# Kernel optimization log

Measured on AMD Instinct MI355X. Metric: run time of the kernel, lower is better.

## Reference

```python
import jax, jax.numpy as jnp
import numpy as np

B, N, M = 2, 2048, 2048
D_K, D_V, H = 256, 256, 8
D_KS = D_K // H  # 32, per-head key dim (ceil(256/8))
D_VS = D_V // H  # 32
MASK_BIG = 1e32


def setup_inputs() -> dict:
    key = jax.random.key(0)
    ks = jax.random.split(key, 10)
    s = 0.02
    queries = jax.random.normal(ks[0], (B, N, D_K), jnp.float32)
    keys_ = jax.random.normal(ks[1], (B, M, D_K), jnp.float32)
    values = jax.random.normal(ks[2], (B, M, D_V), jnp.float32)
    presence = (jax.random.uniform(ks[3], (B, M)) > 0.3).astype(jnp.float32)
    Wq = jax.random.normal(ks[4], (D_K, D_KS * H), jnp.float32) * s
    bq = jnp.zeros((D_KS * H,), jnp.float32)
    Wk = jax.random.normal(ks[5], (D_K, D_KS * H), jnp.float32) * s
    bk = jnp.zeros((D_KS * H,), jnp.float32)
    Wv = jax.random.normal(ks[6], (D_V, D_VS * H), jnp.float32) * s
    bv = jnp.zeros((D_VS * H,), jnp.float32)
    Wo = jax.random.normal(ks[7], (D_VS * H, D_V), jnp.float32) * s
    bo = jnp.zeros((D_V,), jnp.float32)
    return {"queries": queries, "keys": keys_, "values": values, "presence": presence,
            "Wq": Wq, "bq": bq, "Wk": Wk, "bk": bk, "Wv": Wv, "bv": bv, "Wo": Wo, "bo": bo}


def reference(queries, keys, values, presence, Wq, bq, Wk, bk, Wv, bv, Wo, bo):
    # Project and split into heads. torch's split(d_k_s,-1)+cat(...,0) puts the
    # head index as the outer batch dim; a [B,N,H,d] reshape is the same math.
    q = (queries @ Wq + bq).reshape(B, N, H, D_KS)
    k = (keys @ Wk + bk).reshape(B, M, H, D_KS)
    v = (values @ Wv + bv).reshape(B, M, H, D_VS)
    # Raw scores, additive presence mask, then scale by sqrt(per-head d_k)
    scores = jnp.einsum('bnhd,bmhd->bhnm', q, k)
    scores = scores - (1.0 - presence)[:, None, None, :] * MASK_BIG
    attn = jax.nn.softmax(scores / np.sqrt(D_KS).astype(np.float32), axis=-1)
    o = jnp.einsum('bhnm,bmhd->bnhd', attn, v).reshape(B, N, H * D_VS)
    return o @ Wo + bo
```

## Files before the change

### kernel.cpp

```cpp
#include <hip/hip_runtime.h>

#define B_ 2
#define N_ 2048
#define M_ 2048
#define D_ 256
#define H_ 8
#define DH_ 32
#define SPLITS 2
#define QSCALE (0.17677669529663689f * 1.4426950408889634f)

typedef __attribute__((ext_vector_type(8))) short short8;
typedef __attribute__((ext_vector_type(4))) float f32x4;
typedef unsigned short u16;
typedef unsigned int u32;

#if __has_builtin(__builtin_amdgcn_exp2f)
#define EXP2 __builtin_amdgcn_exp2f
#else
#define EXP2 exp2f
#endif

__device__ __forceinline__ u16 f2bf(float f) {
  u32 u = __float_as_uint(f);
  return (u16)((u + 0x7fffu + ((u >> 16) & 1u)) >> 16);
}
__device__ __forceinline__ u32 cvtpk_bf16(float lo, float hi) {
  u32 r;
  asm("v_cvt_pk_bf16_f32 %0, %1, %2" : "=v"(r) : "v"(lo), "v"(hi));
  return r;
}
__device__ __forceinline__ void gload_lds16(const u16* g, u16* l) {
  __builtin_amdgcn_global_load_lds((const __attribute__((address_space(1))) void*)g,
                                   (__attribute__((address_space(3))) void*)l, 16, 0, 0);
}

__global__ __launch_bounds__(256, 2) void qkvproj_kernel(
    const float* __restrict__ Xq, const float* __restrict__ Xk, const float* __restrict__ Xv,
    const float* __restrict__ Wq, const float* __restrict__ Wk, const float* __restrict__ Wv,
    const float* __restrict__ bq, const float* __restrict__ bk, const float* __restrict__ bv,
    u16* __restrict__ qb, u16* __restrict__ kb, u16* __restrict__ vtb) {
  __shared__ u16 wsT[64 * 256];
  __shared__ u16 xs[64 * 256];
  const int p = blockIdx.y;
  const int nb = blockIdx.x & 63, cb = blockIdx.x >> 6;
  const int n0B = nb * 64, c0B = cb * 64;
  const float* X = p == 0 ? Xq : (p == 1 ? Xk : Xv);
  const float* W = p == 0 ? Wq : (p == 1 ? Wk : Wv);
  const float* bias = p == 0 ? bq : (p == 1 ? bk : bv);
  const int t = threadIdx.x;

  {
    const int cL = (t & 15) * 4, kB = (t >> 4) * 16;
    const float* wp = W + (size_t)kB * D_ + c0B + cL;
#pragma unroll
    for (int u = 0; u < 4; ++u) {
      const int k0 = kB + 4 * u;
      const f32x4 w0 = *(const f32x4*)(wp + (size_t)(4 * u + 0) * D_);
      const f32x4 w1 = *(const f32x4*)(wp + (size_t)(4 * u + 1) * D_);
      const f32x4 w2 = *(const f32x4*)(wp + (size_t)(4 * u + 2) * D_);
      const f32x4 w3 = *(const f32x4*)(wp + (size_t)(4 * u + 3) * D_);
#pragma unroll
      for (int cc = 0; cc < 4; ++cc) {
        const int c = cL + cc;
        uint2 v;
        v.x = cvtpk_bf16(w0[cc], w1[cc]);
        v.y = cvtpk_bf16(w2[cc], w3[cc]);
        *(uint2*)(wsT + c * 256 + (((k0 >> 3) ^ (c & 7)) * 8) + (k0 & 7)) = v;
      }
    }
  }
  {
    const int nL = t >> 2, k64 = (t & 3) * 64;
    const float* xp = X + (size_t)(n0B + nL) * D_ + k64;
#pragma unroll
    for (int m = 0; m < 8; ++m) {
      const f32x4 a = *(const f32x4*)(xp + 8 * m);
      const f32x4 b = *(const f32x4*)(xp + 8 * m + 4);
      uint4 v;
      v.x = cvtpk_bf16(a[0], a[1]);
      v.y = cvtpk_bf16(a[2], a[3]);
      v.z = cvtpk_bf16(b[0], b[1]);
      v.w = cvtpk_bf16(b[2], b[3]);
      const int k0 = k64 + 8 * m;
      *(uint4*)(xs + nL * 256 + (((k0 >> 3) ^ (nL & 7)) * 8)) = v;
    }
  }
  __syncthreads();

  const int wv = t >> 6, lane = t & 63, lr = lane & 15, lg = lane >> 4;
  const f32x4 zz = {0.f, 0.f, 0.f, 0.f};
  f32x4 acc[4] = {zz, zz, zz, zz};
  const int arow = wv * 16 + lr;
#pragma unroll
  for (int ks = 0; ks < 8; ++ks) {
    const short8 a = *(const short8*)(wsT + arow * 256 + (((ks * 4 + lg) ^ (arow & 7)) * 8));
#pragma unroll
    for (int ng = 0; ng < 4; ++ng) {
      const int brow = ng * 16 + lr;
      const short8 b = *(const short8*)(xs + brow * 256 + (((ks * 4 + lg) ^ (brow & 7)) * 8));
      acc[ng] = __builtin_amdgcn_mfma_f32_16x16x32_bf16(a, b, acc[ng], 0, 0, 0);
    }
  }

  const int cg4 = c0B + wv * 16 + lg * 4;
  const f32x4 bias4 = *(const f32x4*)(bias + cg4);
  if (p < 2) {
    u16* ob = p == 0 ? qb : kb;
    const float sc = p == 0 ? QSCALE : 1.0f;
#pragma unroll
    for (int ng = 0; ng < 4; ++ng) {
      const int n = n0B + ng * 16 + lr;
      const int b = n >> 11, nn = n & (N_ - 1);
#pragma unroll
      for (int j = 0; j < 4; ++j) {
        const int c = cg4 + j;
        ob[((size_t)(b * H_ + (c >> 5)) * N_ + nn) * DH_ + (c & 31)] =
            f2bf((acc[ng][j] + bias4[j]) * sc);
      }
    }
  } else {
#pragma unroll
    for (int ng = 0; ng < 4; ++ng) {
      const int n = n0B + ng * 16 + lr;
      const int b = n >> 11, nn = n & (M_ - 1);
#pragma unroll
      for (int j = 0; j < 4; ++j) {
        const int c = cg4 + j;
        vtb[((size_t)(b * H_ + (c >> 5)) * DH_ + (c & 31)) * M_ + nn] =
            f2bf(acc[ng][j] + bias4[j]);
      }
    }
  }
}

__global__ __launch_bounds__(512, 4) void attn_kernel(
    const u16* __restrict__ qb, const u16* __restrict__ kb,
    const u16* __restrict__ vtb, const float* __restrict__ presence,
    float* __restrict__ opart, float* __restrict__ lpart) {
  __shared__ u16 kvlds[2][4096];
  __shared__ u16 plds[8][2][1024];
  const int tid = threadIdx.x;
  const int wv = tid >> 6, lane = tid & 63;
  const int lr = lane & 15, lg = lane >> 4;
  const int s = blockIdx.x >> 8;
  const int bh = (blockIdx.x >> 4) & 15;
  const int qblk = blockIdx.x & 15;
  const int b = bh >> 3, h = bh & 7;
  const int n0 = qblk * 128 + wv * 16;
  const int m0 = s * (M_ / SPLITS);
  const int NI = (M_ / SPLITS) / 64;

  const u16* sptr;
  size_t sstep;
  if (wv < 4) {
    const int key = wv * 16 + (lane >> 2);
    const int gs = (lane & 3) ^ ((key >> 1) & 3);
    sptr = kb + ((size_t)bh * M_ + m0 + key) * DH_ + gs * 8;
    sstep = (size_t)64 * DH_;
  } else {
    const int d = (wv - 4) * 8 + (lane >> 3);
    const int gs = (lane & 7) ^ (d & 7);
    sptr = vtb + ((size_t)bh * DH_ + d) * M_ + m0 + gs * 8;
    sstep = 64;
  }
  u16* const ldsw = (u16*)((char*)kvlds + wv * 1024);

  const int ko0 = lr * 32 + (lg ^ ((lr >> 1) & 3)) * 8;
  const int sw = lr & 7;
  const int vo0 = lr * 64 + (lg ^ sw) * 8;
  const int vo1 = lr * 64 + ((4 + lg) ^ sw) * 8;

  const short8 qf = *(const short8*)(qb + ((size_t)bh * N_ + n0 + lr) * DH_ + lg * 8);
  const float* pbase = presence + (size_t)b * M_ + m0 + lg * 4;
  u16* const plw0 = &plds[wv][0][0] + lr * 64;
  u16* const plw1 = &plds[wv][1][0] + lr * 64;

  const f32x4 zz = {0.f, 0.f, 0.f, 0.f};
  f32x4 o0 = zz, o1 = zz, racc = zz;
  short8 vp0, vp1, vp2, vp3;

  gload_lds16(sptr, ldsw);
  __syncthreads();

#pragma unroll 2
  for (int i = 0; i < NI; ++i) {
    const int mm = i * 64;
    const u16* kl = &kvlds[i & 1][0];
    const u16* vl = &kvlds[i & 1][2048];
    f32x4 pr[4];
#pragma unroll
    for (int t = 0; t < 4; ++t) pr[t] = *(const f32x4*)(pbase + mm + t * 16);
    if (i + 1 < NI)
      gload_lds16(sptr + (size_t)(i + 1) * sstep, (u16*)((char*)ldsw + ((i + 1) & 1) * 8192));

    f32x4 s4[4];
#pragma unroll
    for (int t = 0; t < 4; ++t) {
      const short8 kf = *(const short8*)(kl + t * 512 + ko0);
      s4[t] = __builtin_amdgcn_mfma_f32_16x16x32_bf16(kf, qf, zz, 0, 0, 0);
    }
    const short8 v0 = *(const short8*)(vl + vo0);
    const short8 v1 = *(const short8*)(vl + vo1);
    const short8 v2 = *(const short8*)(vl + 1024 + vo0);
    const short8 v3 = *(const short8*)(vl + 1024 + vo1);

    u16* const plw = (i & 1) ? plw1 : plw0;
#pragma unroll
    for (int t = 0; t < 4; ++t) {
      s4[t] += (pr[t] - 1.f) * 1e30f;
#pragma unroll
      for (int j = 0; j < 4; ++j) s4[t][j] = EXP2(s4[t][j]);
      racc += s4[t];
      const int slot = (2 * t + (lg >> 1)) ^ sw;
      *(uint2*)(plw + slot * 8 + (lg & 1) * 4) =
          make_uint2(cvtpk_bf16(s4[t][0], s4[t][1]), cvtpk_bf16(s4[t][2], s4[t][3]));
    }
    if (i > 0) {
      u16* const plr = (i & 1) ? plw0 : plw1;
      const short8 pf0 = *(const short8*)(plr + (lg ^ sw) * 8);
      const short8 pf1 = *(const short8*)(plr + ((4 + lg) ^ sw) * 8);
      o0 = __builtin_amdgcn_mfma_f32_16x16x32_bf16(pf0, vp0, o0, 0, 0, 0);
      o0 = __builtin_amdgcn_mfma_f32_16x16x32_bf16(pf1, vp1, o0, 0, 0, 0);
      o1 = __builtin_amdgcn_mfma_f32_16x16x32_bf16(pf0, vp2, o1, 0, 0, 0);
      o1 = __builtin_amdgcn_mfma_f32_16x16x32_bf16(pf1, vp3, o1, 0, 0, 0);
    }
    vp0 = v0; vp1 = v1; vp2 = v2; vp3 = v3;
    __syncthreads();
  }
  {
    u16* const plr = plw1;
    const short8 pf0 = *(const short8*)(plr + (lg ^ sw) * 8);
    const short8 pf1 = *(const short8*)(plr + ((4 + lg) ^ sw) * 8);
    o0 = __builtin_amdgcn_mfma_f32_16x16x32_bf16(pf0, vp0, o0, 0, 0, 0);
    o0 = __builtin_amdgcn_mfma_f32_16x16x32_bf16(pf1, vp1, o0, 0, 0, 0);
    o1 = __builtin_amdgcn_mfma_f32_16x16x32_bf16(pf0, vp2, o1, 0, 0, 0);
    o1 = __builtin_amdgcn_mfma_f32_16x16x32_bf16(pf1, vp3, o1, 0, 0, 0);
  }

  float l = (racc[0] + racc[1]) + (racc[2] + racc[3]);
  l += __shfl_xor(l, 16);
  l += __shfl_xor(l, 32);
  if (lg == 0) lpart[((size_t)s * (B_ * N_) + b * N_ + n0 + lr) * H_ + h] = l;

  float* ob = opart + ((size_t)s * (B_ * N_) + (size_t)b * N_ + n0) * D_ + h * DH_;
#pragma unroll
  for (int j = 0; j < 4; ++j) {
    const int q = lg * 4 + j;
    ob[(size_t)q * D_ + lr] = o0[j];
    ob[(size_t)q * D_ + 16 + lr] = o1[j];
  }
}

__global__ __launch_bounds__(256, 2) void projo_kernel(
    const float* __restrict__ opart, const float* __restrict__ lpart,
    const float* __restrict__ Wo, const float* __restrict__ bo,
    float* __restrict__ out) {
  __shared__ u16 wsT[64 * 256];
  __shared__ u16 xs[64 * 256];
  const int nb = blockIdx.x & 63, cb = blockIdx.x >> 6;
  const int n0B = nb * 64, c0B = cb * 64;
  const int t = threadIdx.x;

  {
    const int cL = (t & 15) * 4, kB = (t >> 4) * 16;
    const float* wp = Wo + (size_t)kB * D_ + c0B + cL;
#pragma unroll
    for (int u = 0; u < 4; ++u) {
      const int k0 = kB + 4 * u;
      const f32x4 w0 = *(const f32x4*)(wp + (size_t)(4 * u + 0) * D_);
      const f32x4 w1 = *(const f32x4*)(wp + (size_t)(4 * u + 1) * D_);
      const f32x4 w2 = *(const f32x4*)(wp + (size_t)(4 * u + 2) * D_);
      const f32x4 w3 = *(const f32x4*)(wp + (size_t)(4 * u + 3) * D_);
#pragma unroll
      for (int cc = 0; cc < 4; ++cc) {
        const int c = cL + cc;
        uint2 v;
        v.x = cvtpk_bf16(w0[cc], w1[cc]);
        v.y = cvtpk_bf16(w2[cc], w3[cc]);
        *(uint2*)(wsT + c * 256 + (((k0 >> 3) ^ (c & 7)) * 8) + (k0 & 7)) = v;
      }
    }
  }
  {
    const int nL = t >> 2, k64 = (t & 3) * 64;
    const int gn = n0B + nL;
    const float* o0p = opart + (size_t)gn * D_ + k64;
    const float* o1p = o0p + (size_t)(B_ * N_) * D_;
    const int h0 = k64 >> 5;
    const float il0 = 1.f / (lpart[(size_t)gn * H_ + h0] +
                             lpart[((size_t)(B_ * N_) + gn) * H_ + h0]);
    const float il1 = 1.f / (lpart[(size_t)gn * H_ + h0 + 1] +
                             lpart[((size_t)(B_ * N_) + gn) * H_ + h0 + 1]);
#pragma unroll
    for (int m = 0; m < 8; ++m) {
      f32x4 a = *(const f32x4*)(o0p + 8 * m) + *(const f32x4*)(o1p + 8 * m);
      f32x4 b = *(const f32x4*)(o0p + 8 * m + 4) + *(const f32x4*)(o1p + 8 * m + 4);
      const float il = (m < 4) ? il0 : il1;
      a *= il;
      b *= il;
      uint4 v;
      v.x = cvtpk_bf16(a[0], a[1]);
      v.y = cvtpk_bf16(a[2], a[3]);
      v.z = cvtpk_bf16(b[0], b[1]);
      v.w = cvtpk_bf16(b[2], b[3]);
      const int k0 = k64 + 8 * m;
      *(uint4*)(xs + nL * 256 + (((k0 >> 3) ^ (nL & 7)) * 8)) = v;
    }
  }
  __syncthreads();

  const int wv = t >> 6, lane = t & 63, lr = lane & 15, lg = lane >> 4;
  const f32x4 zz = {0.f, 0.f, 0.f, 0.f};
  f32x4 acc[4] = {zz, zz, zz, zz};
  const int arow = wv * 16 + lr;
#pragma unroll
  for (int ks = 0; ks < 8; ++ks) {
    const short8 a = *(const short8*)(xs + arow * 256 + (((ks * 4 + lg) ^ (arow & 7)) * 8));
#pragma unroll
    for (int ng = 0; ng < 4; ++ng) {
      const int brow = ng * 16 + lr;
      const short8 bfr = *(const short8*)(wsT + brow * 256 + (((ks * 4 + lg) ^ (brow & 7)) * 8));
      acc[ng] = __builtin_amdgcn_mfma_f32_16x16x32_bf16(a, bfr, acc[ng], 0, 0, 0);
    }
  }
#pragma unroll
  for (int ng = 0; ng < 4; ++ng) {
    const int c = c0B + ng * 16 + lr;
    const float bb = bo[c];
#pragma unroll
    for (int j = 0; j < 4; ++j)
      out[(size_t)(n0B + wv * 16 + lg * 4 + j) * D_ + c] = acc[ng][j] + bb;
  }
}

extern "C" void kernel_launch(void* const* d_in, const int* in_sizes, int n_in,
                              void* d_out, int out_size, void* d_ws, size_t ws_size,
                              hipStream_t stream) {
  (void)in_sizes; (void)n_in; (void)out_size; (void)ws_size;
  const float* queries  = (const float*)d_in[0];
  const float* keys     = (const float*)d_in[1];
  const float* values   = (const float*)d_in[2];
  const float* presence = (const float*)d_in[3];
  const float* Wq = (const float*)d_in[4];
  const float* bq = (const float*)d_in[5];
  const float* Wk = (const float*)d_in[6];
  const float* bk = (const float*)d_in[7];
  const float* Wv = (const float*)d_in[8];
  const float* bv = (const float*)d_in[9];
  const float* Wo = (const float*)d_in[10];
  const float* bo = (const float*)d_in[11];

  u16* qb  = (u16*)d_ws;
  u16* kb  = qb + (size_t)B_ * H_ * N_ * DH_;
  u16* vtb = kb + (size_t)B_ * H_ * M_ * DH_;
  float* opart = (float*)(vtb + (size_t)B_ * H_ * DH_ * M_);
  float* lpart = opart + (size_t)SPLITS * B_ * N_ * D_;

  qkvproj_kernel<<<dim3(256, 3), 256, 0, stream>>>(
      queries, keys, values, Wq, Wk, Wv, bq, bk, bv, qb, kb, vtb);
  attn_kernel<<<SPLITS * 16 * 16, 512, 0, stream>>>(qb, kb, vtb, presence, opart, lpart);
  projo_kernel<<<256, 256, 0, stream>>>(opart, lpart, Wo, bo, (float*)d_out);
}
```

Baseline: 49.37 us.

## Use 256-thread attention blocks with 64 queries and simpler P·V schedule

Shrinks attention blocks from 8 waves (128 queries) to 4 waves (64 queries) and doubles the grid. Each thread now loads both K and V tiles to LDS, and the P buffer is single-buffered per wave. The software-pipelined P·V that deferred one iteration is replaced by an in-iteration P·V. s_setprio brackets are added around the MFMA groups. This aims for better occupancy and scheduling, but each block loads half as many queries per K/V tile, so K/V reuse drops and global/LDS load traffic per query rises.

```diff
diff --git a/kernel.cpp b/kernel.cpp
--- a/kernel.cpp
+++ b/kernel.cpp
@@ -133,53 +133,44 @@
   }
 }
 
-__global__ __launch_bounds__(512, 4) void attn_kernel(
+__global__ __launch_bounds__(256, 4) void attn_kernel(
     const u16* __restrict__ qb, const u16* __restrict__ kb,
     const u16* __restrict__ vtb, const float* __restrict__ presence,
     float* __restrict__ opart, float* __restrict__ lpart) {
   __shared__ u16 kvlds[2][4096];
-  __shared__ u16 plds[8][2][1024];
-  const int tid = threadIdx.x;
-  const int wv = tid >> 6, lane = tid & 63;
+  __shared__ u16 plds[4][1024];
+  const int t = threadIdx.x;
+  const int wv = t >> 6, lane = t & 63;
   const int lr = lane & 15, lg = lane >> 4;
-  const int s = blockIdx.x >> 8;
-  const int bh = (blockIdx.x >> 4) & 15;
-  const int qblk = blockIdx.x & 15;
+  const int s = blockIdx.x >> 9;
+  const int bh = (blockIdx.x >> 5) & 15;
+  const int qblk = blockIdx.x & 31;
   const int b = bh >> 3, h = bh & 7;
-  const int n0 = qblk * 128 + wv * 16;
+  const int n0 = qblk * 64 + wv * 16;
   const int m0 = s * (M_ / SPLITS);
   const int NI = (M_ / SPLITS) / 64;
 
-  const u16* sptr;
-  size_t sstep;
-  if (wv < 4) {
-    const int key = wv * 16 + (lane >> 2);
-    const int gs = (lane & 3) ^ ((key >> 1) & 3);
-    sptr = kb + ((size_t)bh * M_ + m0 + key) * DH_ + gs * 8;
-    sstep = (size_t)64 * DH_;
-  } else {
-    const int d = (wv - 4) * 8 + (lane >> 3);
-    const int gs = (lane & 7) ^ (d & 7);
-    sptr = vtb + ((size_t)bh * DH_ + d) * M_ + m0 + gs * 8;
-    sstep = 64;
-  }
-  u16* const ldsw = (u16*)((char*)kvlds + wv * 1024);
+  const int gsk = (t & 3) ^ ((t >> 3) & 3);
+  const u16* kst = kb + ((size_t)bh * M_ + m0 + (t >> 2)) * DH_ + gsk * 8;
+  const int gsv = (t & 7) ^ ((t >> 3) & 7);
+  const u16* vst = vtb + ((size_t)bh * DH_ + (t >> 3)) * M_ + m0 + gsv * 8;
+  u16* const ldswK = &kvlds[0][0] + wv * 512;
+  u16* const ldswV = &kvlds[0][0] + 2048 + wv * 512;
 
   const int ko0 = lr * 32 + (lg ^ ((lr >> 1) & 3)) * 8;
   const int sw = lr & 7;
-  const int vo0 = lr * 64 + (lg ^ sw) * 8;
-  const int vo1 = lr * 64 + ((4 + lg) ^ sw) * 8;
+  const int vo0 = (lg ^ sw) * 8;
+  const int vo1 = ((4 + lg) ^ sw) * 8;
 
   const short8 qf = *(const short8*)(qb + ((size_t)bh * N_ + n0 + lr) * DH_ + lg * 8);
   const float* pbase = presence + (size_t)b * M_ + m0 + lg * 4;
-  u16* const plw0 = &plds[wv][0][0] + lr * 64;
-  u16* const plw1 = &plds[wv][1][0] + lr * 64;
+  u16* const plw = plds[wv] + lr * 64;
 
   const f32x4 zz = {0.f, 0.f, 0.f, 0.f};
   f32x4 o0 = zz, o1 = zz, racc = zz;
-  short8 vp0, vp1, vp2, vp3;
-
-  gload_lds16(sptr, ldsw);
+
+  gload_lds16(kst, ldswK);
+  gload_lds16(vst, ldswV);
   __syncthreads();
 
 #pragma unroll 2
@@ -189,52 +180,45 @@
     const u16* vl = &kvlds[i & 1][2048];
     f32x4 pr[4];
 #pragma unroll
-    for (int t = 0; t < 4; ++t) pr[t] = *(const f32x4*)(pbase + mm + t * 16);
-    if (i + 1 < NI)
-      gload_lds16(sptr + (size_t)(i + 1) * sstep, (u16*)((char*)ldsw + ((i + 1) & 1) * 8192));
+    for (int tt = 0; tt < 4; ++tt) pr[tt] = *(const f32x4*)(pbase + mm + tt * 16);
+    if (i + 1 < NI) {
+      const int bo = ((i + 1) & 1) * 4096;
+      gload_lds16(kst + (size_t)(i + 1) * (64 * DH_), ldswK + bo);
+      gload_lds16(vst + (size_t)(i + 1) * 64, ldswV + bo);
+    }
 
     f32x4 s4[4];
-#pragma unroll
-    for (int t = 0; t < 4; ++t) {
-      const short8 kf = *(const short8*)(kl + t * 512 + ko0);
-      s4[t] = __builtin_amdgcn_mfma_f32_16x16x32_bf16(kf, qf, zz, 0, 0, 0);
-    }
-    const short8 v0 = *(const short8*)(vl + vo0);
-    const short8 v1 = *(const short8*)(vl + vo1);
-    const short8 v2 = *(const short8*)(vl + 1024 + vo0);
-    const short8 v3 = *(const short8*)(vl + 1024 + vo1);
-
-    u16* const plw = (i & 1) ? plw1 : plw0;
-#pragma unroll
-    for (int t = 0; t < 4; ++t) {
-      s4[t] += (pr[t] - 1.f) * 1e30f;
-#pragma unroll
-      for (int j = 0; j < 4; ++j) s4[t][j] = EXP2(s4[t][j]);
-      racc += s4[t];
-      const int slot = (2 * t + (lg >> 1)) ^ sw;
+    __builtin_amdgcn_s_setprio(1);
+#pragma unroll
+    for (int tt = 0; tt < 4; ++tt) {
+      const short8 kf = *(const short8*)(kl + tt * 512 + ko0);
+      s4[tt] = __builtin_amdgcn_mfma_f32_16x16x32_bf16(kf, qf, zz, 0, 0, 0);
+    }
+    __builtin_amdgcn_s_setprio(0);
+
+#pragma unroll
+    for (int tt = 0; tt < 4; ++tt) {
+      s4[tt] += (pr[tt] - 1.f) * 1e30f;
+#pragma unroll
+      for (int j = 0; j < 4; ++j) s4[tt][j] = EXP2(s4[tt][j]);
+      racc += s4[tt];
+      const int slot = (2 * tt + (lg >> 1)) ^ sw;
       *(uint2*)(plw + slot * 8 + (lg & 1) * 4) =
-          make_uint2(cvtpk_bf16(s4[t][0], s4[t][1]), cvtpk_bf16(s4[t][2], s4[t][3]));
-    }
-    if (i > 0) {
-      u16* const plr = (i & 1) ? plw0 : plw1;
-      const short8 pf0 = *(const short8*)(plr + (lg ^ sw) * 8);
-      const short8 pf1 = *(const short8*)(plr + ((4 + lg) ^ sw) * 8);
-      o0 = __builtin_amdgcn_mfma_f32_16x16x32_bf16(pf0, vp0, o0, 0, 0, 0);
-      o0 = __builtin_amdgcn_mfma_f32_16x16x32_bf16(pf1, vp1, o0, 0, 0, 0);
-      o1 = __builtin_amdgcn_mfma_f32_16x16x32_bf16(pf0, vp2, o1, 0, 0, 0);
-      o1 = __builtin_amdgcn_mfma_f32_16x16x32_bf16(pf1, vp3, o1, 0, 0, 0);
-    }
-    vp0 = v0; vp1 = v1; vp2 = v2; vp3 = v3;
+          make_uint2(cvtpk_bf16(s4[tt][0], s4[tt][1]), cvtpk_bf16(s4[tt][2], s4[tt][3]));
+    }
+    const short8 pf0 = *(const short8*)(plw + vo0);
+    const short8 pf1 = *(const short8*)(plw + vo1);
+    const short8 vf0 = *(const short8*)(vl + lr * 64 + vo0);
+    const short8 vf1 = *(const short8*)(vl + lr * 64 + vo1);
+    const short8 vf2 = *(const short8*)(vl + (16 + lr) * 64 + vo0);
+    const short8 vf3 = *(const short8*)(vl + (16 + lr) * 64 + vo1);
+    __builtin_amdgcn_s_setprio(1);
+    o0 = __builtin_amdgcn_mfma_f32_16x16x32_bf16(pf0, vf0, o0, 0, 0, 0);
+    o0 = __builtin_amdgcn_mfma_f32_16x16x32_bf16(pf1, vf1, o0, 0, 0, 0);
+    o1 = __builtin_amdgcn_mfma_f32_16x16x32_bf16(pf0, vf2, o1, 0, 0, 0);
+    o1 = __builtin_amdgcn_mfma_f32_16x16x32_bf16(pf1, vf3, o1, 0, 0, 0);
+    __builtin_amdgcn_s_setprio(0);
     __syncthreads();
-  }
-  {
-    u16* const plr = plw1;
-    const short8 pf0 = *(const short8*)(plr + (lg ^ sw) * 8);
-    const short8 pf1 = *(const short8*)(plr + ((4 + lg) ^ sw) * 8);
-    o0 = __builtin_amdgcn_mfma_f32_16x16x32_bf16(pf0, vp0, o0, 0, 0, 0);
-    o0 = __builtin_amdgcn_mfma_f32_16x16x32_bf16(pf1, vp1, o0, 0, 0, 0);
-    o1 = __builtin_amdgcn_mfma_f32_16x16x32_bf16(pf0, vp2, o1, 0, 0, 0);
-    o1 = __builtin_amdgcn_mfma_f32_16x16x32_bf16(pf1, vp3, o1, 0, 0, 0);
   }
 
   float l = (racc[0] + racc[1]) + (racc[2] + racc[3]);
@@ -358,6 +342,6 @@
 
   qkvproj_kernel<<<dim3(256, 3), 256, 0, stream>>>(
       queries, keys, values, Wq, Wk, Wv, bq, bk, bv, qb, kb, vtb);
-  attn_kernel<<<SPLITS * 16 * 16, 512, 0, stream>>>(qb, kb, vtb, presence, opart, lpart);
+  attn_kernel<<<SPLITS * 16 * 32, 256, 0, stream>>>(qb, kb, vtb, presence, opart, lpart);
   projo_kernel<<<256, 256, 0, stream>>>(opart, lpart, Wo, bo, (float*)d_out);
 }
```

Result: faster. 47.57 us (-3.7%).
